# Optimization experiments

Measured on AMD Instinct MI355X. Metric: run time of the kernel, lower is better.

Reference implementation:

```python
import jax, jax.numpy as jnp
import numpy as np

B, D, U1, U2 = 16384, 512, 512, 512
BN_EPS = 1e-3  # keras BatchNormalization default epsilon


def sparsemax(z):
    # z: [..., D]; standard sparsemax along last axis (Martins & Astudillo)
    d = z.shape[-1]
    z_sorted = -jnp.sort(-z, axis=-1)                      # descending
    z_cum = jnp.cumsum(z_sorted, axis=-1)
    k = jnp.arange(1, d + 1, dtype=z.dtype)
    support = (1.0 + k * z_sorted) > z_cum                 # [..., D] bool
    k_z = jnp.sum(support, axis=-1, keepdims=True)         # support size
    tau = (jnp.take_along_axis(z_cum, k_z.astype(jnp.int32) - 1, axis=-1) - 1.0) / k_z.astype(z.dtype)
    return jnp.maximum(z - tau, 0.0)


def setup_inputs() -> dict:
    key = jax.random.key(0)
    ks = jax.random.split(key, 8)
    x = jax.random.normal(ks[0], (B, D), dtype=jnp.float32)
    W1 = jax.random.normal(ks[1], (D, U1), dtype=jnp.float32) * 0.05
    b1 = jnp.zeros((U1,), jnp.float32)
    centers = jax.random.normal(ks[2], (U2, D), dtype=jnp.float32)      # paraboloid centers
    coefs = jax.random.normal(ks[3], (U2, D), dtype=jnp.float32) * 0.1  # paraboloid axis coefficients
    bn_gamma = jnp.ones((D,), jnp.float32)
    bn_beta = jnp.zeros((D,), jnp.float32)
    bn_mean = jnp.zeros((D,), jnp.float32)
    bn_var = jnp.ones((D,), jnp.float32)
    W_out = jax.random.normal(ks[4], (U1 + U2, D), dtype=jnp.float32) * 0.05
    b_out = jnp.zeros((D,), jnp.float32)
    w_add = jnp.array([0.5, 0.5], jnp.float32)  # WeightedAdd learnable scalars
    return {"x": x, "W1": W1, "b1": b1, "centers": centers, "coefs": coefs,
            "bn_gamma": bn_gamma, "bn_beta": bn_beta, "bn_mean": bn_mean, "bn_var": bn_var,
            "W_out": W_out, "b_out": b_out, "w_add": w_add}


def reference(x, W1, b1, centers, coefs, bn_gamma, bn_beta, bn_mean, bn_var, W_out, b_out, w_add):
    # Dense branch
    h1 = jax.nn.relu(x @ W1 + b1)                               # [B, U1]
    # BoundedParaboloids branch: BatchNorm (inference stats) then bounded paraboloids
    xb = (x - bn_mean) * jax.lax.rsqrt(bn_var + BN_EPS) * bn_gamma + bn_beta
    # q_j = sum_d (coefs[j,d] * (xb_d - centers[j,d]))^2, computed via GEMMs
    A = coefs * coefs                                            # [U2, D]
    q = (xb * xb) @ A.T - 2.0 * (xb @ (A * centers).T) + jnp.sum(A * centers * centers, axis=-1)
    h2 = jax.nn.relu(1.0 - q)                                    # [B, U2] bounded paraboloids
    # Output embedding: Dense(relu) on concat
    emb = jax.nn.relu(jnp.concatenate([h1, h2], axis=-1) @ W_out + b_out)  # [B, D]
    # WeightedAdd of (dropout-identity) inputs and embedding; dropout_rate=0 / inference
    pre = w_add[0] * x + w_add[1] * emb
    mask = sparsemax(pre)                                        # [B, D]
    return mask
```

## Files before the change

kernel.cpp:

```cpp
#include <hip/hip_runtime.h>
#include <math.h>

typedef float f4 __attribute__((ext_vector_type(4)));
typedef float f32x4 __attribute__((ext_vector_type(4)));
typedef __bf16 bf16x8 __attribute__((ext_vector_type(8)));
typedef unsigned short u16;
typedef u16 us8 __attribute__((ext_vector_type(8)));

__device__ __forceinline__ u16 f2bf(float f) {
  unsigned u = __builtin_bit_cast(unsigned, f);
  unsigned r = u + 0x7fffu + ((u >> 16) & 1u);
  return (u16)(r >> 16);
}
__device__ __forceinline__ float bf2f(u16 h) {
  unsigned u = ((unsigned)h) << 16;
  return __builtin_bit_cast(float, u);
}

__global__ __launch_bounds__(256) void prep_bn_kernel(
    const float* __restrict__ gamma, const float* __restrict__ beta,
    const float* __restrict__ mean, const float* __restrict__ var,
    float* __restrict__ scale, float* __restrict__ shift) {
  int d = blockIdx.x * blockDim.x + threadIdx.x;
  if (d < 512) {
    float s = rsqrtf(var[d] + 1e-3f) * gamma[d];
    scale[d] = s;
    shift[d] = beta[d] - mean[d] * s;
  }
}

__global__ __launch_bounds__(64) void prep_params_kernel(
    const float* __restrict__ coefs, const float* __restrict__ centers,
    u16* __restrict__ pth, float* __restrict__ cvec) {
  int j = blockIdx.x;
  int l = threadIdx.x;
  int d0 = l * 8;
  f4 c0 = *(const f4*)(coefs + (size_t)j * 512 + d0);
  f4 c1 = *(const f4*)(coefs + (size_t)j * 512 + d0 + 4);
  f4 e0 = *(const f4*)(centers + (size_t)j * 512 + d0);
  f4 e1 = *(const f4*)(centers + (size_t)j * 512 + d0 + 4);
  us8 pa, pb;
  float acc = 0.f;
#pragma unroll
  for (int e = 0; e < 8; ++e) {
    float cf = (e < 4) ? c0[e] : c1[e - 4];
    float ce = (e < 4) ? e0[e] : e1[e - 4];
    float a = cf * cf;
    pa[e] = f2bf(a);
    pb[e] = f2bf(-2.f * a * ce);
    acc = fmaf(a * ce, ce, acc);
  }
  *(us8*)(pth + (size_t)j * 1024 + d0) = pa;
  *(us8*)(pth + (size_t)j * 1024 + 512 + d0) = pb;
#pragma unroll
  for (int off = 32; off; off >>= 1) acc += __shfl_xor(acc, off);
  if (l == 0) cvec[j] = acc;
}

__global__ __launch_bounds__(256) void transpose_split_kernel(
    const float* __restrict__ in, u16* __restrict__ th, int K, int N) {
  __shared__ float t[32][33];
  int lx = threadIdx.x;
  int ly = threadIdx.y;
  int n0 = blockIdx.x * 32, k0 = blockIdx.y * 32;
#pragma unroll
  for (int i = 0; i < 4; ++i)
    t[ly + 8 * i][lx] = in[(size_t)(k0 + ly + 8 * i) * N + n0 + lx];
  __syncthreads();
#pragma unroll
  for (int i = 0; i < 4; ++i) {
    float v = t[lx][ly + 8 * i];
    th[(size_t)(n0 + ly + 8 * i) * K + k0 + lx] = f2bf(v);
  }
}

__global__ __launch_bounds__(256) void conv_x_kernel(
    const float* __restrict__ x, const float* __restrict__ scale,
    const float* __restrict__ shift, u16* __restrict__ xh,
    u16* __restrict__ xb, u16* __restrict__ xsq) {
  int gid = blockIdx.x * 256 + threadIdx.x;
  int m = gid >> 6;
  int d0 = (gid & 63) * 8;
  f4 v0 = *(const f4*)(x + (size_t)m * 512 + d0);
  f4 v1 = *(const f4*)(x + (size_t)m * 512 + d0 + 4);
  f4 s0 = *(const f4*)(scale + d0);
  f4 s1 = *(const f4*)(scale + d0 + 4);
  f4 h0 = *(const f4*)(shift + d0);
  f4 h1 = *(const f4*)(shift + d0 + 4);
  us8 oh, ob, oq;
#pragma unroll
  for (int e = 0; e < 8; ++e) {
    float xv = (e < 4) ? v0[e] : v1[e - 4];
    float sc = (e < 4) ? s0[e] : s1[e - 4];
    float sh = (e < 4) ? h0[e] : h1[e - 4];
    oh[e] = f2bf(xv);
    float xbf = fmaf(xv, sc, sh);
    ob[e] = f2bf(xbf);
    oq[e] = f2bf(xbf * xbf);
  }
  *(us8*)(xh + (size_t)m * 512 + d0) = oh;
  *(us8*)(xb + (size_t)m * 512 + d0) = ob;
  *(us8*)(xsq + (size_t)m * 512 + d0) = oq;
}

__global__ __launch_bounds__(256, 2) void gemm_fused12(
    const u16* __restrict__ Xh, const u16* __restrict__ Xb,
    const u16* __restrict__ Xsq, const u16* __restrict__ W1th,
    const u16* __restrict__ Pth, const float* __restrict__ b1,
    const float* __restrict__ cvec, u16* __restrict__ Hout) {
  extern __shared__ char smem[];
  const int tid = threadIdx.x;
  const int l = tid & 63;
  const int w = tid >> 6;
  const int wm = w & 1, wn = w >> 1;
  const int lr = l & 15, lk = l >> 4;
  const int sx = lr & 7;
  const int bid = blockIdx.x;
  const int L = (bid & 7) * 128 + (bid >> 3);
  const int p = L >> 3;
  const int g = ((L >> 2) & 1) ^ 1;
  const int n = L & 3;
  const int m0 = p * 128, n0 = n * 128;
  const int Kg = g ? 1024 : 512;
  const int nt = g ? 16 : 8;
  const u16* Bmat = g ? Pth : W1th;
  const int srow = l >> 3;
  const int sslot = (l & 7) ^ srow;

  f32x4 acc[4][4];
#pragma unroll
  for (int i = 0; i < 4; ++i)
#pragma unroll
    for (int j = 0; j < 4; ++j) acc[i][j] = (f32x4){0.f, 0.f, 0.f, 0.f};

#define F12_STAGE(buf, k0)                                                    \
  {                                                                           \
    const u16* Asrc = g ? (((k0) < 512) ? Xsq : Xb) : Xh;                     \
    const int kb = (k0)&511;                                                  \
    char* dA = smem + (buf)*16384;                                            \
    char* dB = smem + 32768 + (buf)*16384;                                    \
    _Pragma("unroll") for (int pp = 0; pp < 4; ++pp) {                        \
      int c = pp * 4 + w;                                                     \
      int row = c * 8 + srow;                                                 \
      int loff = c * 1024;                                                    \
      size_t goa = (size_t)(m0 + row) * 512 + kb + sslot * 8;                 \
      size_t gob = (size_t)(n0 + row) * Kg + (k0) + sslot * 8;                \
      __builtin_amdgcn_global_load_lds(                                       \
          (const __attribute__((address_space(1))) void*)(Asrc + goa),        \
          (__attribute__((address_space(3))) void*)(dA + loff), 16, 0, 0);    \
      __builtin_amdgcn_global_load_lds(                                       \
          (const __attribute__((address_space(1))) void*)(Bmat + gob),        \
          (__attribute__((address_space(3))) void*)(dB + loff), 16, 0, 0);    \
    }                                                                         \
  }

  F12_STAGE(0, 0);
  __syncthreads();
  for (int t = 0; t < nt; ++t) {
    if (t + 1 < nt) F12_STAGE((t + 1) & 1, (t + 1) * 64);
    const char* sA = smem + (t & 1) * 16384;
    const char* sB = smem + 32768 + (t & 1) * 16384;
#pragma unroll
    for (int ks = 0; ks < 2; ++ks) {
      bf16x8 av[4], bv[4];
#pragma unroll
      for (int i = 0; i < 4; ++i)
        av[i] = *(const bf16x8*)(sA + (wm * 64 + i * 16 + lr) * 128 +
                                 (((ks * 4 + lk) ^ sx) * 16));
#pragma unroll
      for (int j = 0; j < 4; ++j)
        bv[j] = *(const bf16x8*)(sB + (wn * 64 + j * 16 + lr) * 128 +
                                 (((ks * 4 + lk) ^ sx) * 16));
#pragma unroll
      for (int i = 0; i < 4; ++i)
#pragma unroll
        for (int j = 0; j < 4; ++j)
          acc[i][j] = __builtin_amdgcn_mfma_f32_16x16x32_bf16(av[i], bv[j],
                                                              acc[i][j], 0, 0, 0);
    }
    __syncthreads();
  }
#undef F12_STAGE

  const int mwb = m0 + wm * 64;
  const int nwb = n0 + wn * 64;
  const float* bias = g ? cvec : b1;
#pragma unroll
  for (int j = 0; j < 4; ++j) {
    int nn = nwb + j * 16 + lr;
    float bv = bias[nn];
#pragma unroll
    for (int i = 0; i < 4; ++i) {
#pragma unroll
      for (int r = 0; r < 4; ++r) {
        int m = mwb + i * 16 + lk * 4 + r;
        float v = acc[i][j][r] + bv;
        v = g ? fmaxf(1.f - v, 0.f) : fmaxf(v, 0.f);
        Hout[(size_t)m * 1024 + g * 512 + nn] = f2bf(v);
      }
    }
  }
}

__global__ __launch_bounds__(256, 2) void gemm3(
    const u16* __restrict__ Ah, const u16* __restrict__ Bh,
    const float* __restrict__ bias, const float* __restrict__ xorig,
    const float* __restrict__ wadd, float* __restrict__ outp) {
  extern __shared__ char smem[];
  const int tid = threadIdx.x;
  const int l = tid & 63;
  const int w = tid >> 6;
  const int wm = w & 1, wn = w >> 1;
  const int lr = l & 15, lk = l >> 4;
  const int sx = lr & 7;
  const int bid = blockIdx.x;
  const int lin = (bid & 7) * 64 + (bid >> 3);
  const int m0 = (lin >> 2) * 128, n0 = (lin & 3) * 128;
  const int srow = l >> 3;
  const int sslot = (l & 7) ^ srow;

  f32x4 acc[4][4];
#pragma unroll
  for (int i = 0; i < 4; ++i)
#pragma unroll
    for (int j = 0; j < 4; ++j) acc[i][j] = (f32x4){0.f, 0.f, 0.f, 0.f};

#define G3_STAGE(buf, k0)                                                     \
  {                                                                           \
    char* dA = smem + (buf)*16384;                                            \
    char* dB = smem + 32768 + (buf)*16384;                                    \
    _Pragma("unroll") for (int pp = 0; pp < 4; ++pp) {                        \
      int c = pp * 4 + w;                                                     \
      int row = c * 8 + srow;                                                 \
      int loff = c * 1024;                                                    \
      size_t gob = (size_t)(n0 + row) * 1024 + (k0) + sslot * 8;              \
      size_t goa = (size_t)(m0 + row) * 1024 + (k0) + sslot * 8;              \
      __builtin_amdgcn_global_load_lds(                                       \
          (const __attribute__((address_space(1))) void*)(Bh + gob),          \
          (__attribute__((address_space(3))) void*)(dB + loff), 16, 0, 0);    \
      __builtin_amdgcn_global_load_lds(                                       \
          (const __attribute__((address_space(1))) void*)(Ah + goa),          \
          (__attribute__((address_space(3))) void*)(dA + loff), 16, 0, 0);    \
    }                                                                         \
  }

  G3_STAGE(0, 0);
  __syncthreads();
  for (int t = 0; t < 16; ++t) {
    if (t + 1 < 16) G3_STAGE((t + 1) & 1, (t + 1) * 64);
    const char* sA = smem + (t & 1) * 16384;
    const char* sB = smem + 32768 + (t & 1) * 16384;
#pragma unroll
    for (int ks = 0; ks < 2; ++ks) {
      bf16x8 av[4], bv[4];
#pragma unroll
      for (int i = 0; i < 4; ++i)
        av[i] = *(const bf16x8*)(sA + (wm * 64 + i * 16 + lr) * 128 +
                                 (((ks * 4 + lk) ^ sx) * 16));
#pragma unroll
      for (int j = 0; j < 4; ++j)
        bv[j] = *(const bf16x8*)(sB + (wn * 64 + j * 16 + lr) * 128 +
                                 (((ks * 4 + lk) ^ sx) * 16));
#pragma unroll
      for (int i = 0; i < 4; ++i)
#pragma unroll
        for (int j = 0; j < 4; ++j)
          acc[i][j] = __builtin_amdgcn_mfma_f32_16x16x32_bf16(av[i], bv[j],
                                                              acc[i][j], 0, 0, 0);
    }
    __syncthreads();
  }
#undef G3_STAGE

  const int mwb = m0 + wm * 64;
  const int nwb = n0 + wn * 64;
  float w0 = wadd[0], w1 = wadd[1];
#pragma unroll
  for (int j = 0; j < 4; ++j) {
    int n = nwb + j * 16 + lr;
    float bv = bias[n];
#pragma unroll
    for (int i = 0; i < 4; ++i) {
#pragma unroll
      for (int r = 0; r < 4; ++r) {
        int m = mwb + i * 16 + lk * 4 + r;
        float v = fmaxf(acc[i][j][r] + bv, 0.f);
        outp[(size_t)m * 512 + n] = fmaf(w1, v, w0 * xorig[(size_t)m * 512 + n]);
      }
    }
  }
}

__global__ __launch_bounds__(256) void sparsemax_kernel(float* __restrict__ out) {
  int row = blockIdx.x * 4 + (threadIdx.x >> 6);
  int lane = threadIdx.x & 63;
  float* rp = out + (size_t)row * 512;
  f4 z0 = *(const f4*)(rp + lane * 8);
  f4 z1 = *(const f4*)(rp + lane * 8 + 4);
  float z[8];
#pragma unroll
  for (int e = 0; e < 4; ++e) {
    z[e] = z0[e];
    z[4 + e] = z1[e];
  }
  float m = z[0];
#pragma unroll
  for (int i = 1; i < 8; ++i) m = fmaxf(m, z[i]);
#pragma unroll
  for (int off = 32; off; off >>= 1) m = fmaxf(m, __shfl_xor(m, off));
  float tau = m - 1.0f;
  for (int it = 0; it < 32; ++it) {
    float s = 0.f, k = 0.f;
#pragma unroll
    for (int i = 0; i < 8; ++i) {
      if (z[i] > tau) {
        s += z[i] - tau;
        k += 1.f;
      }
    }
#pragma unroll
    for (int off = 32; off; off >>= 1) {
      s += __shfl_xor(s, off);
      k += __shfl_xor(k, off);
    }
    if (k < 0.5f) break;
    float tn = tau + (s - 1.f) / k;
    if (tn == tau) break;
    tau = tn;
  }
  float s = 0.f, k = 0.f;
#pragma unroll
  for (int i = 0; i < 8; ++i)
    if (z[i] > tau) {
      s += z[i];
      k += 1.f;
    }
#pragma unroll
  for (int off = 32; off; off >>= 1) {
    s += __shfl_xor(s, off);
    k += __shfl_xor(k, off);
  }
  float tauf = (k >= 0.5f) ? (s - 1.f) / k : (m - 1.f);
  f4 o0, o1;
#pragma unroll
  for (int e = 0; e < 4; ++e) {
    o0[e] = fmaxf(z[e] - tauf, 0.f);
    o1[e] = fmaxf(z[4 + e] - tauf, 0.f);
  }
  *(f4*)(rp + lane * 8) = o0;
  *(f4*)(rp + lane * 8 + 4) = o1;
}

extern "C" void kernel_launch(void* const* d_in, const int* in_sizes, int n_in,
                              void* d_out, int out_size, void* d_ws,
                              size_t ws_size, hipStream_t stream) {
  const float* x = (const float*)d_in[0];
  const float* W1 = (const float*)d_in[1];
  const float* b1 = (const float*)d_in[2];
  const float* centers = (const float*)d_in[3];
  const float* coefs = (const float*)d_in[4];
  const float* gamma = (const float*)d_in[5];
  const float* beta = (const float*)d_in[6];
  const float* mean = (const float*)d_in[7];
  const float* var = (const float*)d_in[8];
  const float* W_out = (const float*)d_in[9];
  const float* b_out = (const float*)d_in[10];
  const float* wadd = (const float*)d_in[11];
  float* out = (float*)d_out;

  char* ws = (char*)d_ws;
  u16* Hh = (u16*)(ws);
  u16* Xh = (u16*)(ws + 33554432);
  u16* Xb = (u16*)(ws + 50331648);
  char* pool = ws + 67108864;
  u16* W1th = (u16*)(pool);
  u16* Pth = (u16*)(pool + 1048576);
  float* cvec = (float*)(ws + 69206016);
  float* scale = (float*)(ws + 69208064);
  float* shift = (float*)(ws + 69210112);
  u16* Xsq = (u16*)d_out;
  const bool bigws = (ws_size >= (size_t)70260736);
  u16* Wth = bigws ? (u16*)(ws + 69212160) : (u16*)(pool);

  prep_bn_kernel<<<2, 256, 0, stream>>>(gamma, beta, mean, var, scale, shift);
  prep_params_kernel<<<512, 64, 0, stream>>>(coefs, centers, Pth, cvec);
  transpose_split_kernel<<<dim3(16, 16), dim3(32, 8), 0, stream>>>(W1, W1th,
                                                                   512, 512);
  if (bigws) {
    transpose_split_kernel<<<dim3(16, 32), dim3(32, 8), 0, stream>>>(
        W_out, Wth, 1024, 512);
  }
  conv_x_kernel<<<4096, 256, 0, stream>>>(x, scale, shift, Xh, Xb, Xsq);

  gemm_fused12<<<1024, 256, 65536, stream>>>(Xh, Xb, Xsq, W1th, Pth, b1, cvec,
                                             Hh);

  if (!bigws) {
    transpose_split_kernel<<<dim3(16, 32), dim3(32, 8), 0, stream>>>(
        W_out, Wth, 1024, 512);
  }
  gemm3<<<512, 256, 65536, stream>>>(Hh, Wth, b_out, x, wadd, out);
  sparsemax_kernel<<<4096, 256, 0, stream>>>(out);
}
```

Measured before the change: 107.7 us.

## Prefetch two stages ahead with vmcnt waits in both GEMMs; remap sparsemax rows

Both bf16 GEMM main loops now issue loads for tiles 0 and 1 up front. Each iteration waits only until the current tile's loads are done (s_waitcnt vmcnt(8) keeps the next tile's 8 loads in flight), then does a raw barrier. The freed buffer is refilled with tile t+2 after the compute barrier, so global-to-LDS loads overlap more compute, using sched_barrier to hold instruction order. The sparsemax kernel also remaps block IDs so that consecutive blocks are spread across XCDs, which may change L2 locality. The hand-placed waitcnt relies on each stage issuing exactly 8 vector memory ops per thread.

```diff
diff --git a/kernel.cpp b/kernel.cpp
--- a/kernel.cpp
+++ b/kernel.cpp
@@ -102,6 +102,15 @@
   *(us8*)(xb + (size_t)m * 512 + d0) = ob;
   *(us8*)(xsq + (size_t)m * 512 + d0) = oq;
 }
+
+__device__ __forceinline__ void wait_vm8() {
+  asm volatile("s_waitcnt vmcnt(8)" ::: "memory");
+}
+__device__ __forceinline__ void wait_vm0() {
+  asm volatile("s_waitcnt vmcnt(0)" ::: "memory");
+}
+__device__ __forceinline__ void sbar() { __builtin_amdgcn_s_barrier(); }
+__device__ __forceinline__ void sgb0() { __builtin_amdgcn_sched_barrier(0); }
 
 __global__ __launch_bounds__(256, 2) void gemm_fused12(
     const u16* __restrict__ Xh, const u16* __restrict__ Xb,
@@ -155,9 +164,16 @@
   }
 
   F12_STAGE(0, 0);
-  __syncthreads();
+  F12_STAGE(1, 64);
   for (int t = 0; t < nt; ++t) {
-    if (t + 1 < nt) F12_STAGE((t + 1) & 1, (t + 1) * 64);
+    if (t + 1 < nt) {
+      wait_vm8();
+    } else {
+      wait_vm0();
+    }
+    sgb0();
+    sbar();
+    sgb0();
     const char* sA = smem + (t & 1) * 16384;
     const char* sB = smem + 32768 + (t & 1) * 16384;
 #pragma unroll
@@ -178,7 +194,10 @@
           acc[i][j] = __builtin_amdgcn_mfma_f32_16x16x32_bf16(av[i], bv[j],
                                                               acc[i][j], 0, 0, 0);
     }
-    __syncthreads();
+    sgb0();
+    sbar();
+    sgb0();
+    if (t + 2 < nt) F12_STAGE(t & 1, (t + 2) * 64);
   }
 #undef F12_STAGE
 
@@ -245,9 +264,16 @@
   }
 
   G3_STAGE(0, 0);
-  __syncthreads();
+  G3_STAGE(1, 64);
   for (int t = 0; t < 16; ++t) {
-    if (t + 1 < 16) G3_STAGE((t + 1) & 1, (t + 1) * 64);
+    if (t + 1 < 16) {
+      wait_vm8();
+    } else {
+      wait_vm0();
+    }
+    sgb0();
+    sbar();
+    sgb0();
     const char* sA = smem + (t & 1) * 16384;
     const char* sB = smem + 32768 + (t & 1) * 16384;
 #pragma unroll
@@ -268,7 +294,10 @@
           acc[i][j] = __builtin_amdgcn_mfma_f32_16x16x32_bf16(av[i], bv[j],
                                                               acc[i][j], 0, 0, 0);
     }
-    __syncthreads();
+    sgb0();
+    sbar();
+    sgb0();
+    if (t + 2 < 16) G3_STAGE(t & 1, (t + 2) * 64);
   }
 #undef G3_STAGE
 
@@ -292,7 +321,8 @@
 }
 
 __global__ __launch_bounds__(256) void sparsemax_kernel(float* __restrict__ out) {
-  int row = blockIdx.x * 4 + (threadIdx.x >> 6);
+  int wrk = (blockIdx.x & 7) * 512 + (blockIdx.x >> 3);
+  int row = wrk * 4 + (threadIdx.x >> 6);
   int lane = threadIdx.x & 63;
   float* rp = out + (size_t)row * 512;
   f4 z0 = *(const f4*)(rp + lane * 8);
```

Result: no change. 106.3 us, median of 2 (-1.3%).
